# Kernel optimization log

Measured on AMD Instinct MI355X. Metric: run time of the kernel, lower is better.

Reference implementation:

```python
import jax, jax.numpy as jnp
import numpy as np

DIM = 2048
N_HEADS = 32
N_KV_HEADS = 8
HEAD_DIM = DIM // N_HEADS  # 64
SEQ = 2048
BATCH = 2


def _rope_freqs(seq_len, head_dim, theta=10000.0):
    inv = 1.0 / (theta ** (np.arange(0, head_dim, 2)[: head_dim // 2].astype(np.float32) / head_dim))
    t = np.arange(seq_len, dtype=np.float32)
    ang = np.outer(t, inv)  # (seq, head_dim//2)
    return jnp.asarray(np.cos(ang)), jnp.asarray(np.sin(ang))


def setup_inputs() -> dict:
    key = jax.random.key(0)
    ks = jax.random.split(key, 5)
    x = jax.random.normal(ks[0], (BATCH, SEQ, DIM), dtype=jnp.float32)
    s = 1.0 / np.sqrt(DIM)
    wq = jax.random.normal(ks[1], (N_HEADS * HEAD_DIM, DIM), dtype=jnp.float32) * s
    wk = jax.random.normal(ks[2], (N_KV_HEADS * HEAD_DIM, DIM), dtype=jnp.float32) * s
    wv = jax.random.normal(ks[3], (N_KV_HEADS * HEAD_DIM, DIM), dtype=jnp.float32) * s
    wo = jax.random.normal(ks[4], (DIM, N_HEADS * HEAD_DIM), dtype=jnp.float32) * s
    freqs_cos, freqs_sin = _rope_freqs(SEQ, HEAD_DIM)
    return {"x": x, "freqs_cos": freqs_cos, "freqs_sin": freqs_sin,
            "wq": wq, "wk": wk, "wv": wv, "wo": wo}


def _apply_rope(t, cos, sin):
    # t: (B, S, H, D); cos/sin: (S, D//2) broadcast to (1, S, 1, D//2)
    B, S, H, D = t.shape
    tr = t.reshape(B, S, H, D // 2, 2)
    x0, x1 = tr[..., 0], tr[..., 1]
    c = cos[None, :, None, :]
    s = sin[None, :, None, :]
    o0 = x0 * c - x1 * s
    o1 = x0 * s + x1 * c
    return jnp.stack([o0, o1], axis=-1).reshape(B, S, H, D)


def reference(x, freqs_cos, freqs_sin, wq, wk, wv, wo):
    B, S, _ = x.shape
    H, KV, D = N_HEADS, N_KV_HEADS, HEAD_DIM
    rep = H // KV
    xq = jnp.einsum('bsd,hd->bsh', x, wq).reshape(B, S, H, D)
    xk = jnp.einsum('bsd,hd->bsh', x, wk).reshape(B, S, KV, D)
    xv = jnp.einsum('bsd,hd->bsh', x, wv).reshape(B, S, KV, D)
    xq = _apply_rope(xq, freqs_cos, freqs_sin)
    xk = _apply_rope(xk, freqs_cos, freqs_sin)
    # GQA without materializing repeated K/V: group q heads as (KV, rep).
    # repeat_interleave on dim=2 maps q head h -> kv head h // rep.
    xqg = xq.reshape(B, S, KV, rep, D)
    scale = 1.0 / jnp.sqrt(jnp.float32(D))
    scores = jnp.einsum('bqkrd,bskd->bkrqs', xqg, xk) * scale  # (B,KV,rep,S,S)
    causal = jnp.tril(jnp.ones((S, S), dtype=bool))
    scores = jnp.where(causal[None, None, None], scores, jnp.float32(-jnp.inf))
    probs = jax.nn.softmax(scores, axis=-1)
    out = jnp.einsum('bkrqs,bskd->bqkrd', probs, xv)  # (B,S,KV,rep,D)
    out = out.reshape(B, S, H * D)
    return jnp.einsum('bsh,dh->bsd', out, wo)
```

## Files before the change

kernel.cpp:

```cpp
#include <hip/hip_runtime.h>

#define DIMSZ 2048
#define NH 32
#define NKV 8
#define HD 64
#define SEQLEN 2048
#define BATCH 2
#define NROWS (BATCH*SEQLEN)
#define NQKVC 3072

typedef __bf16 bf16x8 __attribute__((ext_vector_type(8)));
typedef __bf16 bf16x2 __attribute__((ext_vector_type(2)));
typedef float f32x4v __attribute__((ext_vector_type(4)));
typedef float f32x2v __attribute__((ext_vector_type(2)));

__device__ __forceinline__ unsigned short f2bf(float f) {
  __bf16 h = (__bf16)f;
  union { __bf16 h; unsigned short u; } v; v.h = h; return v.u;
}
__device__ __forceinline__ unsigned int pk2bf(float lo, float hi) {
  f32x2v v; v[0] = lo; v[1] = hi;
  bf16x2 h = __builtin_convertvector(v, bf16x2);
  union { bf16x2 h; unsigned int u; } c; c.h = h; return c.u;
}
__device__ __forceinline__ float bf2f(unsigned int bits16) {
  union { unsigned int u; float f; } v; v.u = bits16 << 16; return v.f;
}
__device__ __forceinline__ int swz128(int row, int colBytes) {
  return row * 128 + (colBytes ^ ((row & 7) << 4));
}

#define GLOAD16(g, l) __builtin_amdgcn_global_load_lds( \
    (const __attribute__((address_space(1))) unsigned int*)(g), \
    (__attribute__((address_space(3))) unsigned int*)(l), 16, 0, 0)

__global__ void k_cvt(const float* __restrict__ s, unsigned short* __restrict__ d, int n4) {
  int i = blockIdx.x * 256 + threadIdx.x;
  if (i >= n4) return;
  float4 v = reinterpret_cast<const float4*>(s)[i];
  uint2 pk; pk.x = pk2bf(v.x, v.y); pk.y = pk2bf(v.z, v.w);
  reinterpret_cast<uint2*>(d)[i] = pk;
}

__global__ void k_cvt_w(const float* __restrict__ wq, const float* __restrict__ wk,
                        const float* __restrict__ wv, unsigned short* __restrict__ d) {
  int i = blockIdx.x * 256 + threadIdx.x;
  const float* s; int off;
  if (i < 1048576)      { s = wq; off = i; }
  else if (i < 1310720) { s = wk; off = i - 1048576; }
  else                  { s = wv; off = i - 1310720; }
  float4 v = reinterpret_cast<const float4*>(s)[off];
  uint2 pk; pk.x = pk2bf(v.x, v.y); pk.y = pk2bf(v.z, v.w);
  reinterpret_cast<uint2*>(d)[i] = pk;
}

template<int OUT_BF16>
__global__ __launch_bounds__(256, 2) void k_gemm_bt(
    const unsigned short* __restrict__ A,
    const unsigned short* __restrict__ B,
    void* __restrict__ Cv, int M, int N, int K)
{
  constexpr int BK = 64;
  __shared__ __attribute__((aligned(16))) unsigned short smA[128 * BK];
  __shared__ __attribute__((aligned(16))) unsigned short smB[128 * BK];
  const int tid = threadIdx.x;
  const int lane = tid & 63;
  const int wid = tid >> 6;
  const int lr = lane & 15, lg = lane >> 4;
  const int gx = gridDim.x;
  int lin = blockIdx.y * gx + blockIdx.x;
  const int cpx = (gx * gridDim.y) >> 3;
  lin = (lin & 7) * cpx + (lin >> 3);
  const int m0 = (lin / gx) * 128, n0 = (lin % gx) * 128;
  const int wr = (wid >> 1) * 64, wc = (wid & 1) * 64;

  f32x4v acc[4][4];
  #pragma unroll
  for (int i = 0; i < 4; i++)
    #pragma unroll
    for (int j = 0; j < 4; j++)
      acc[i][j] = f32x4v{0.f, 0.f, 0.f, 0.f};

  for (int k0 = 0; k0 < K; k0 += BK) {
    #pragma unroll
    for (int c = 0; c < 4; c++) {
      const int chunk = wid * 4 + c;
      const int idx = chunk * 64 + lane;
      const int row = idx >> 3, s = idx & 7;
      const int ks = (s ^ (row & 7)) * 8;
      GLOAD16(A + (size_t)(m0 + row) * K + k0 + ks, &smA[chunk * 512]);
      GLOAD16(B + (size_t)(n0 + row) * K + k0 + ks, &smB[chunk * 512]);
    }
    __syncthreads();
    #pragma unroll
    for (int ks = 0; ks < 2; ks++) {
      bf16x8 af[4], bfv[4];
      #pragma unroll
      for (int m = 0; m < 4; m++)
        af[m] = *reinterpret_cast<const bf16x8*>((char*)smA + swz128(wr + m * 16 + lr, ks * 64 + lg * 16));
      #pragma unroll
      for (int n = 0; n < 4; n++)
        bfv[n] = *reinterpret_cast<const bf16x8*>((char*)smB + swz128(wc + n * 16 + lr, ks * 64 + lg * 16));
      #pragma unroll
      for (int m = 0; m < 4; m++)
        #pragma unroll
        for (int n = 0; n < 4; n++)
          acc[m][n] = __builtin_amdgcn_mfma_f32_16x16x32_bf16(af[m], bfv[n], acc[m][n], 0, 0, 0);
    }
    __syncthreads();
  }
  #pragma unroll
  for (int m = 0; m < 4; m++)
    #pragma unroll
    for (int n = 0; n < 4; n++)
      #pragma unroll
      for (int r = 0; r < 4; r++) {
        const size_t row = m0 + wr + m * 16 + lg * 4 + r;
        const size_t col = n0 + wc + n * 16 + lr;
        if (OUT_BF16) ((unsigned short*)Cv)[row * N + col] = f2bf(acc[m][n][r]);
        else          ((float*)Cv)[row * N + col] = acc[m][n][r];
      }
}

__global__ void k_rope_q(const unsigned short* __restrict__ qkv,
                         const float* __restrict__ fc, const float* __restrict__ fs,
                         unsigned short* __restrict__ Qb)
{
  const int tid = blockIdx.x * 256 + threadIdx.x;
  const int i = tid & 31;
  const int t2 = tid >> 5;
  const int h = t2 & 31;
  const int row = t2 >> 5;
  const int s = row & (SEQLEN - 1);
  const int b = row >> 11;
  const unsigned int u = *reinterpret_cast<const unsigned int*>(qkv + (size_t)row * NQKVC + h * HD + 2 * i);
  const float x0 = bf2f(u & 0xffffu), x1 = bf2f(u >> 16);
  const float c = fc[s * 32 + i], sn = fs[s * 32 + i];
  const float SCL = 0.18033688011112043f;
  const float o0 = (x0 * c - x1 * sn) * SCL;
  const float o1 = (x0 * sn + x1 * c) * SCL;
  *reinterpret_cast<unsigned int*>(Qb + ((size_t)((b * NH + h) * SEQLEN + s)) * HD + 2 * i) = pk2bf(o0, o1);
}

__global__ void k_rope_k(const unsigned short* __restrict__ qkv,
                         const float* __restrict__ fc, const float* __restrict__ fs,
                         unsigned short* __restrict__ Kb)
{
  const int tid = blockIdx.x * 256 + threadIdx.x;
  const int i = tid & 31;
  const int t2 = tid >> 5;
  const int kv = t2 & 7;
  const int row = t2 >> 3;
  const int s = row & (SEQLEN - 1);
  const int b = row >> 11;
  const unsigned int u = *reinterpret_cast<const unsigned int*>(
      qkv + (size_t)row * NQKVC + DIMSZ + kv * HD + 2 * i);
  const float x0 = bf2f(u & 0xffffu), x1 = bf2f(u >> 16);
  const float c = fc[s * 32 + i], sn = fs[s * 32 + i];
  const float o0 = x0 * c - x1 * sn;
  const float o1 = x0 * sn + x1 * c;
  *reinterpret_cast<unsigned int*>(Kb + ((size_t)((b * NKV + kv) * SEQLEN + s)) * HD + 2 * i) = pk2bf(o0, o1);
}

__global__ void k_vt(const unsigned short* __restrict__ qkv, unsigned short* __restrict__ Vt) {
  __shared__ unsigned short tile[64][72];
  const int st = blockIdx.x, kv = blockIdx.y, b = blockIdx.z;
  const int tid = threadIdx.x;
  #pragma unroll
  for (int j2 = 0; j2 < 2; j2++) {
    const int s = (tid >> 3) + j2 * 32, dc = (tid & 7) * 8;
    const int row = b * SEQLEN + st * 64 + s;
    uint4 v = *reinterpret_cast<const uint4*>(
        qkv + (size_t)row * NQKVC + DIMSZ + NKV * HD + kv * HD + dc);
    const unsigned short* vs = reinterpret_cast<const unsigned short*>(&v);
    #pragma unroll
    for (int j = 0; j < 8; j++) tile[s][dc + j] = vs[j];
  }
  __syncthreads();
  {
    const int d = tid >> 2, sc = (tid & 3) * 16;
    unsigned short tmp[16];
    #pragma unroll
    for (int j = 0; j < 16; j++) tmp[j] = tile[sc + j][d];
    unsigned short* outp = Vt + ((size_t)((b * NKV + kv) * HD) + d) * SEQLEN + st * 64 + sc;
    *reinterpret_cast<uint4*>(outp)     = *reinterpret_cast<uint4*>(tmp);
    *reinterpret_cast<uint4*>(outp + 8) = *reinterpret_cast<uint4*>(tmp + 8);
  }
}

__global__ __launch_bounds__(512, 2) void k_attn(
    const unsigned short* __restrict__ Qg,
    const unsigned short* __restrict__ Kg,
    const unsigned short* __restrict__ Vt,
    unsigned short* __restrict__ Og)
{
  constexpr int KVB = 64;
  __shared__ __attribute__((aligned(16))) unsigned short sK0[KVB * HD];
  __shared__ __attribute__((aligned(16))) unsigned short sK1[KVB * HD];
  __shared__ __attribute__((aligned(16))) unsigned short sV0[HD * KVB];
  __shared__ __attribute__((aligned(16))) unsigned short sV1[HD * KVB];
  __shared__ __attribute__((aligned(16))) unsigned short sP[8 * 16 * KVB];
  const int tid = threadIdx.x;
  const int lane = tid & 63, wid = tid >> 6;
  const int lr = lane & 15, lg = lane >> 4;
  const int orig = blockIdx.x;
  const int w = (orig & 7) * 64 + (orig >> 3);
  const int kvh = w >> 6;
  const int b = (w >> 5) & 1;
  const int h = kvh * 4 + ((w >> 3) & 3);
  const int qp = w & 7;
  const unsigned short* Qp = Qg + ((size_t)(b * NH + h) * SEQLEN) * HD;
  const unsigned short* Kp = Kg + ((size_t)(b * NKV + kvh) * SEQLEN) * HD;
  const unsigned short* Vp = Vt + ((size_t)(b * NKV + kvh) * HD) * SEQLEN;
  unsigned short* Pw = sP + wid * (16 * KVB);

  const int sidx = wid * 64 + lane;
  const int srow = sidx >> 3;
  const int scol = ((sidx & 7) ^ (srow & 7)) * 8;

  for (int phase = 0; phase < 2; phase++) {
    const int qt = phase ? (15 - qp) : qp;
    const int qrow0 = qt * 128 + wid * 16;
    bf16x8 aq[2];
    #pragma unroll
    for (int ks = 0; ks < 2; ks++)
      aq[ks] = *reinterpret_cast<const bf16x8*>(Qp + (size_t)(qrow0 + lr) * HD + ks * 32 + lg * 8);

    f32x4v accO[4];
    #pragma unroll
    for (int r = 0; r < 4; r++) accO[r] = f32x4v{0.f, 0.f, 0.f, 0.f};
    float mrun = -3.0e38f, lrun = 0.f;

    auto compute = [&](int kv0, auto& sKb, auto& sVb) {
      if (kv0 > qrow0 + 15) return;
      f32x4v sfr[4];
      #pragma unroll
      for (int c = 0; c < 4; c++) sfr[c] = f32x4v{0.f, 0.f, 0.f, 0.f};
      __builtin_amdgcn_s_setprio(1);
      #pragma unroll
      for (int ks = 0; ks < 2; ks++) {
        bf16x8 bk[4];
        #pragma unroll
        for (int c = 0; c < 4; c++)
          bk[c] = *reinterpret_cast<const bf16x8*>((char*)sKb + swz128(c * 16 + lr, ks * 64 + lg * 16));
        #pragma unroll
        for (int c = 0; c < 4; c++)
          sfr[c] = __builtin_amdgcn_mfma_f32_16x16x32_bf16(bk[c], aq[ks], sfr[c], 0, 0, 0);
      }
      __builtin_amdgcn_s_setprio(0);
      if (kv0 + KVB - 1 > qrow0) {
        const int q = qrow0 + lr;
        #pragma unroll
        for (int c = 0; c < 4; c++)
          #pragma unroll
          for (int r = 0; r < 4; r++) {
            const int kv = kv0 + c * 16 + lg * 4 + r;
            if (kv > q) sfr[c][r] = -1.0e30f;
          }
      }
      float mc[4];
      #pragma unroll
      for (int c = 0; c < 4; c++)
        mc[c] = fmaxf(fmaxf(sfr[c][0], sfr[c][1]), fmaxf(sfr[c][2], sfr[c][3]));
      float tm = fmaxf(fmaxf(mc[0], mc[1]), fmaxf(mc[2], mc[3]));
      tm = fmaxf(tm, __shfl_xor(tm, 16));
      tm = fmaxf(tm, __shfl_xor(tm, 32));
      const float mo = mrun;
      const bool defer = __all(tm <= mo + 8.0f);
      const float mn = defer ? mo : fmaxf(mo, tm);
      float rc[4];
      #pragma unroll
      for (int c = 0; c < 4; c++) {
        float p0 = __builtin_amdgcn_exp2f(sfr[c][0] - mn);
        float p1 = __builtin_amdgcn_exp2f(sfr[c][1] - mn);
        float p2 = __builtin_amdgcn_exp2f(sfr[c][2] - mn);
        float p3 = __builtin_amdgcn_exp2f(sfr[c][3] - mn);
        sfr[c][0] = p0; sfr[c][1] = p1; sfr[c][2] = p2; sfr[c][3] = p3;
        rc[c] = (p0 + p1) + (p2 + p3);
      }
      float rs = (rc[0] + rc[1]) + (rc[2] + rc[3]);
      rs += __shfl_xor(rs, 16);
      rs += __shfl_xor(rs, 32);
      if (defer) {
        lrun += rs;
      } else {
        const float sc = __builtin_amdgcn_exp2f(mo - mn);
        mrun = mn;
        lrun = lrun * sc + rs;
        #pragma unroll
        for (int r = 0; r < 4; r++) {
          const float scr = __shfl(sc, (lg << 4) + (lg << 2) + r);
          #pragma unroll
          for (int dc = 0; dc < 4; dc++) accO[dc][r] *= scr;
        }
      }
      #pragma unroll
      for (int c = 0; c < 4; c++) {
        uint2 pk;
        pk.x = pk2bf(sfr[c][0], sfr[c][1]);
        pk.y = pk2bf(sfr[c][2], sfr[c][3]);
        *reinterpret_cast<uint2*>((char*)Pw + swz128(lr, c * 32 + lg * 8)) = pk;
      }
      __builtin_amdgcn_s_setprio(1);
      #pragma unroll
      for (int ks = 0; ks < 2; ks++) {
        bf16x8 ap = *reinterpret_cast<const bf16x8*>((char*)Pw + swz128(lr, ks * 64 + lg * 16));
        bf16x8 bv[4];
        #pragma unroll
        for (int dc = 0; dc < 4; dc++)
          bv[dc] = *reinterpret_cast<const bf16x8*>((char*)sVb + swz128(dc * 16 + lr, ks * 64 + lg * 16));
        #pragma unroll
        for (int dc = 0; dc < 4; dc++)
          accO[dc] = __builtin_amdgcn_mfma_f32_16x16x32_bf16(ap, bv[dc], accO[dc], 0, 0, 0);
      }
      __builtin_amdgcn_s_setprio(0);
    };

    const int nt = qt * 2 + 2;
    GLOAD16(Kp + (size_t)srow * HD + scol, &sK0[wid * 512]);
    GLOAD16(Vp + (size_t)srow * SEQLEN + scol, &sV0[wid * 512]);
    __syncthreads();
    for (int t = 0; t < nt; t += 2) {
      {
        const int kn = (t + 1) * KVB;
        GLOAD16(Kp + (size_t)(kn + srow) * HD + scol, &sK1[wid * 512]);
        GLOAD16(Vp + (size_t)srow * SEQLEN + kn + scol, &sV1[wid * 512]);
      }
      compute(t * KVB, sK0, sV0);
      __syncthreads();
      if (t + 2 < nt) {
        const int kn = (t + 2) * KVB;
        GLOAD16(Kp + (size_t)(kn + srow) * HD + scol, &sK0[wid * 512]);
        GLOAD16(Vp + (size_t)srow * SEQLEN + kn + scol, &sV0[wid * 512]);
      }
      compute((t + 1) * KVB, sK1, sV1);
      __syncthreads();
    }
    const float inv = 1.0f / lrun;
    #pragma unroll
    for (int r = 0; r < 4; r++) {
      const float invr = __shfl(inv, (lg << 4) + (lg << 2) + r);
      const int q = qrow0 + lg * 4 + r;
      #pragma unroll
      for (int dc = 0; dc < 4; dc++) {
        const int d = dc * 16 + lr;
        Og[(size_t)(b * SEQLEN + q) * DIMSZ + h * HD + d] = f2bf(accO[dc][r] * invr);
      }
    }
  }
}

extern "C" void kernel_launch(void* const* d_in, const int* in_sizes, int n_in,
                              void* d_out, int out_size, void* d_ws, size_t ws_size,
                              hipStream_t stream)
{
  const float* x  = (const float*)d_in[0];
  const float* fc = (const float*)d_in[1];
  const float* fs = (const float*)d_in[2];
  const float* wq = (const float*)d_in[3];
  const float* wk = (const float*)d_in[4];
  const float* wv = (const float*)d_in[5];
  const float* wo = (const float*)d_in[6];
  float* out = (float*)d_out;
  char* ws = (char*)d_ws;

  unsigned short* xb    = (unsigned short*)(ws + 0);
  unsigned short* wqkvb = (unsigned short*)(ws + 16777216);
  unsigned short* wob   = (unsigned short*)(ws + 29360128);
  unsigned short* qkv   = (unsigned short*)(ws + 37748736);
  unsigned short* Qb    = (unsigned short*)(ws + 62914560);
  unsigned short* Kb    = (unsigned short*)(ws + 79691776);
  unsigned short* Vtb   = (unsigned short*)(ws + 83886080);
  unsigned short* attnb = (unsigned short*)(ws + 88080384);

  k_cvt<<<8192, 256, 0, stream>>>(x,  xb, 2097152);
  k_cvt_w<<<6144, 256, 0, stream>>>(wq, wk, wv, wqkvb);
  k_cvt<<<4096, 256, 0, stream>>>(wo, wob, 1048576);

  dim3 g1(24, 32);
  k_gemm_bt<1><<<g1, 256, 0, stream>>>(xb, wqkvb, qkv, NROWS, NQKVC, DIMSZ);

  k_rope_q<<<16384, 256, 0, stream>>>(qkv, fc, fs, Qb);
  k_rope_k<<<4096, 256, 0, stream>>>(qkv, fc, fs, Kb);
  dim3 gv(32, 8, 2);
  k_vt<<<gv, 256, 0, stream>>>(qkv, Vtb);

  k_attn<<<512, 512, 0, stream>>>(Qb, Kb, Vtb, attnb);

  dim3 g2(16, 32);
  k_gemm_bt<0><<<g2, 256, 0, stream>>>(attnb, wob, out, NROWS, DIMSZ, DIMSZ);
}
```

Measured before the change: 186.5 us.

## Fuse RoPE, Q scaling and V transpose into the QKV GEMM epilogue

Adds a dedicated QKV projection GEMM whose epilogue applies rotary embedding and the softmax scale to Q and K. It pairs adjacent columns with a lane shuffle and writes directly into head-major Q/K buffers, while V tiles are written transposed into the Vt layout. This removes the intermediate qkv buffer round trip and three separate elementwise/transpose kernel launches. In exchange the epilogue does scattered 2-byte stores and per-element cos/sin loads, which may be less coalesced than the old dedicated kernels.

Result: faster. 175.3 us (-6.0%).

```diff
diff --git a/kernel.cpp b/kernel.cpp
--- a/kernel.cpp
+++ b/kernel.cpp
@@ -52,6 +52,108 @@
   float4 v = reinterpret_cast<const float4*>(s)[off];
   uint2 pk; pk.x = pk2bf(v.x, v.y); pk.y = pk2bf(v.z, v.w);
   reinterpret_cast<uint2*>(d)[i] = pk;
+}
+
+__global__ __launch_bounds__(256, 2) void k_gemm_qkv(
+    const unsigned short* __restrict__ A,
+    const unsigned short* __restrict__ B,
+    const float* __restrict__ fc, const float* __restrict__ fs,
+    unsigned short* __restrict__ Qb, unsigned short* __restrict__ Kb,
+    unsigned short* __restrict__ Vt)
+{
+  constexpr int BK = 64, K = DIMSZ, N = NQKVC;
+  __shared__ __attribute__((aligned(16))) unsigned short smA[128 * BK];
+  __shared__ __attribute__((aligned(16))) unsigned short smB[128 * BK];
+  const int tid = threadIdx.x;
+  const int lane = tid & 63;
+  const int wid = tid >> 6;
+  const int lr = lane & 15, lg = lane >> 4;
+  const int gx = gridDim.x;
+  int lin = blockIdx.y * gx + blockIdx.x;
+  const int cpx = (gx * gridDim.y) >> 3;
+  lin = (lin & 7) * cpx + (lin >> 3);
+  const int m0 = (lin / gx) * 128, n0 = (lin % gx) * 128;
+  const int wr = (wid >> 1) * 64, wc = (wid & 1) * 64;
+
+  f32x4v acc[4][4];
+  #pragma unroll
+  for (int i = 0; i < 4; i++)
+    #pragma unroll
+    for (int j = 0; j < 4; j++)
+      acc[i][j] = f32x4v{0.f, 0.f, 0.f, 0.f};
+
+  for (int k0 = 0; k0 < K; k0 += BK) {
+    #pragma unroll
+    for (int c = 0; c < 4; c++) {
+      const int chunk = wid * 4 + c;
+      const int idx = chunk * 64 + lane;
+      const int row = idx >> 3, s = idx & 7;
+      const int ks = (s ^ (row & 7)) * 8;
+      GLOAD16(A + (size_t)(m0 + row) * K + k0 + ks, &smA[chunk * 512]);
+      GLOAD16(B + (size_t)(n0 + row) * K + k0 + ks, &smB[chunk * 512]);
+    }
+    __syncthreads();
+    #pragma unroll
+    for (int ks = 0; ks < 2; ks++) {
+      bf16x8 af[4], bfv[4];
+      #pragma unroll
+      for (int m = 0; m < 4; m++)
+        af[m] = *reinterpret_cast<const bf16x8*>((char*)smA + swz128(wr + m * 16 + lr, ks * 64 + lg * 16));
+      #pragma unroll
+      for (int n = 0; n < 4; n++)
+        bfv[n] = *reinterpret_cast<const bf16x8*>((char*)smB + swz128(wc + n * 16 + lr, ks * 64 + lg * 16));
+      #pragma unroll
+      for (int m = 0; m < 4; m++)
+        #pragma unroll
+        for (int n = 0; n < 4; n++)
+          acc[m][n] = __builtin_amdgcn_mfma_f32_16x16x32_bf16(af[m], bfv[n], acc[m][n], 0, 0, 0);
+    }
+    __syncthreads();
+  }
+  const int bx = n0 >> 7;
+  if (bx < 20) {
+    const bool isQ = bx < 16;
+    const float SCL = isQ ? 0.18033688011112043f : 1.0f;
+    #pragma unroll
+    for (int n = 0; n < 4; n++) {
+      const int col = n0 + wc + n * 16 + lr;
+      const int d = col & 63;
+      const int i = d >> 1;
+      const float sgn = (d & 1) ? 1.0f : -1.0f;
+      unsigned short* dst;
+      if (isQ) dst = Qb + (size_t)(col >> 6) * (SEQLEN * HD) + d;
+      else     dst = Kb + (size_t)((col - 2048) >> 6) * (SEQLEN * HD) + d;
+      #pragma unroll
+      for (int m = 0; m < 4; m++)
+        #pragma unroll
+        for (int r = 0; r < 4; r++) {
+          const int row = m0 + wr + m * 16 + lg * 4 + r;
+          const int s = row & (SEQLEN - 1), b = row >> 11;
+          const float v = acc[m][n][r];
+          const float p = __shfl_xor(v, 1);
+          const float c = fc[s * 32 + i], sn = fs[s * 32 + i];
+          const float o = (v * c + sgn * p * sn) * SCL;
+          const size_t headStride = (size_t)(isQ ? NH : NKV) * SEQLEN * HD;
+          dst[(size_t)b * headStride + (size_t)s * HD] = f2bf(o);
+        }
+    }
+  } else {
+    #pragma unroll
+    for (int n = 0; n < 4; n++) {
+      const int col = n0 + wc + n * 16 + lr;
+      const int kvh = (col - 2560) >> 6, d = col & 63;
+      #pragma unroll
+      for (int m = 0; m < 4; m++) {
+        const int row0 = m0 + wr + m * 16 + lg * 4;
+        const int s0 = row0 & (SEQLEN - 1), b = row0 >> 11;
+        uint2 pk;
+        pk.x = pk2bf(acc[m][n][0], acc[m][n][1]);
+        pk.y = pk2bf(acc[m][n][2], acc[m][n][3]);
+        *reinterpret_cast<uint2*>(
+            Vt + ((size_t)((b * NKV + kvh) * HD) + d) * SEQLEN + s0) = pk;
+      }
+    }
+  }
 }
 
 template<int OUT_BF16>
@@ -120,72 +222,6 @@
         if (OUT_BF16) ((unsigned short*)Cv)[row * N + col] = f2bf(acc[m][n][r]);
         else          ((float*)Cv)[row * N + col] = acc[m][n][r];
       }
-}
-
-__global__ void k_rope_q(const unsigned short* __restrict__ qkv,
-                         const float* __restrict__ fc, const float* __restrict__ fs,
-                         unsigned short* __restrict__ Qb)
-{
-  const int tid = blockIdx.x * 256 + threadIdx.x;
-  const int i = tid & 31;
-  const int t2 = tid >> 5;
-  const int h = t2 & 31;
-  const int row = t2 >> 5;
-  const int s = row & (SEQLEN - 1);
-  const int b = row >> 11;
-  const unsigned int u = *reinterpret_cast<const unsigned int*>(qkv + (size_t)row * NQKVC + h * HD + 2 * i);
-  const float x0 = bf2f(u & 0xffffu), x1 = bf2f(u >> 16);
-  const float c = fc[s * 32 + i], sn = fs[s * 32 + i];
-  const float SCL = 0.18033688011112043f;
-  const float o0 = (x0 * c - x1 * sn) * SCL;
-  const float o1 = (x0 * sn + x1 * c) * SCL;
-  *reinterpret_cast<unsigned int*>(Qb + ((size_t)((b * NH + h) * SEQLEN + s)) * HD + 2 * i) = pk2bf(o0, o1);
-}
-
-__global__ void k_rope_k(const unsigned short* __restrict__ qkv,
-                         const float* __restrict__ fc, const float* __restrict__ fs,
-                         unsigned short* __restrict__ Kb)
-{
-  const int tid = blockIdx.x * 256 + threadIdx.x;
-  const int i = tid & 31;
-  const int t2 = tid >> 5;
-  const int kv = t2 & 7;
-  const int row = t2 >> 3;
-  const int s = row & (SEQLEN - 1);
-  const int b = row >> 11;
-  const unsigned int u = *reinterpret_cast<const unsigned int*>(
-      qkv + (size_t)row * NQKVC + DIMSZ + kv * HD + 2 * i);
-  const float x0 = bf2f(u & 0xffffu), x1 = bf2f(u >> 16);
-  const float c = fc[s * 32 + i], sn = fs[s * 32 + i];
-  const float o0 = x0 * c - x1 * sn;
-  const float o1 = x0 * sn + x1 * c;
-  *reinterpret_cast<unsigned int*>(Kb + ((size_t)((b * NKV + kv) * SEQLEN + s)) * HD + 2 * i) = pk2bf(o0, o1);
-}
-
-__global__ void k_vt(const unsigned short* __restrict__ qkv, unsigned short* __restrict__ Vt) {
-  __shared__ unsigned short tile[64][72];
-  const int st = blockIdx.x, kv = blockIdx.y, b = blockIdx.z;
-  const int tid = threadIdx.x;
-  #pragma unroll
-  for (int j2 = 0; j2 < 2; j2++) {
-    const int s = (tid >> 3) + j2 * 32, dc = (tid & 7) * 8;
-    const int row = b * SEQLEN + st * 64 + s;
-    uint4 v = *reinterpret_cast<const uint4*>(
-        qkv + (size_t)row * NQKVC + DIMSZ + NKV * HD + kv * HD + dc);
-    const unsigned short* vs = reinterpret_cast<const unsigned short*>(&v);
-    #pragma unroll
-    for (int j = 0; j < 8; j++) tile[s][dc + j] = vs[j];
-  }
-  __syncthreads();
-  {
-    const int d = tid >> 2, sc = (tid & 3) * 16;
-    unsigned short tmp[16];
-    #pragma unroll
-    for (int j = 0; j < 16; j++) tmp[j] = tile[sc + j][d];
-    unsigned short* outp = Vt + ((size_t)((b * NKV + kv) * HD) + d) * SEQLEN + st * 64 + sc;
-    *reinterpret_cast<uint4*>(outp)     = *reinterpret_cast<uint4*>(tmp);
-    *reinterpret_cast<uint4*>(outp + 8) = *reinterpret_cast<uint4*>(tmp + 8);
-  }
 }
 
 __global__ __launch_bounds__(512, 2) void k_attn(
@@ -367,7 +403,6 @@
   unsigned short* xb    = (unsigned short*)(ws + 0);
   unsigned short* wqkvb = (unsigned short*)(ws + 16777216);
   unsigned short* wob   = (unsigned short*)(ws + 29360128);
-  unsigned short* qkv   = (unsigned short*)(ws + 37748736);
   unsigned short* Qb    = (unsigned short*)(ws + 62914560);
   unsigned short* Kb    = (unsigned short*)(ws + 79691776);
   unsigned short* Vtb   = (unsigned short*)(ws + 83886080);
@@ -378,12 +413,7 @@
   k_cvt<<<4096, 256, 0, stream>>>(wo, wob, 1048576);
 
   dim3 g1(24, 32);
-  k_gemm_bt<1><<<g1, 256, 0, stream>>>(xb, wqkvb, qkv, NROWS, NQKVC, DIMSZ);
-
-  k_rope_q<<<16384, 256, 0, stream>>>(qkv, fc, fs, Qb);
-  k_rope_k<<<4096, 256, 0, stream>>>(qkv, fc, fs, Kb);
-  dim3 gv(32, 8, 2);
-  k_vt<<<gv, 256, 0, stream>>>(qkv, Vtb);
+  k_gemm_qkv<<<g1, 256, 0, stream>>>(xb, wqkvb, fc, fs, Qb, Kb, Vtb);
 
   k_attn<<<512, 512, 0, stream>>>(Qb, Kb, Vtb, attnb);
 
```
